# Optimization experiments

Measured on AMD Instinct MI355X. Metric: run time of the kernel, lower is better.

## Reference

```python
import jax, jax.numpy as jnp
import numpy as np

B, S, D, H, FF = 2, 2048, 1024, 16, 4096
DH = D // H
EPS = 1e-5


def rmsnorm(x, g):
    rms = jnp.sqrt(jnp.mean(x * x, axis=-1, keepdims=True) + EPS)
    return x / rms * g


def gelu(x):
    return x * 0.5 * (1.0 + jax.lax.erf(x / np.float32(np.sqrt(2.0))))


def setup_inputs() -> dict:
    key = jax.random.key(0)
    ks = jax.random.split(key, 9)
    sd = np.float32(1.0 / np.sqrt(D))
    sf = np.float32(1.0 / np.sqrt(FF))
    return {
        'x': jax.random.normal(ks[0], (B, S, D), jnp.float32),
        'wq': jax.random.normal(ks[1], (D, D), jnp.float32) * sd,
        'wk': jax.random.normal(ks[2], (D, D), jnp.float32) * sd,
        'wv': jax.random.normal(ks[3], (D, D), jnp.float32) * sd,
        'wo': jax.random.normal(ks[4], (D, D), jnp.float32) * sd,
        'w1': jax.random.normal(ks[5], (FF, D), jnp.float32) * sd,
        'w2': jax.random.normal(ks[6], (D, FF), jnp.float32) * sf,
        'g1': jax.random.uniform(ks[7], (D,), jnp.float32),
        'g2': jax.random.uniform(ks[8], (D,), jnp.float32),
    }


def reference(x, wq, wk, wv, wo, w1, w2, g1, g2):
    b, s, d = x.shape
    h = rmsnorm(x, g1)
    # torch Linear: y = x @ W.T ; split heads -> [b, s, H, DH]
    q = jnp.einsum('bsd,ed->bse', h, wq).reshape(b, s, H, DH)
    k = jnp.einsum('bsd,ed->bse', h, wk).reshape(b, s, H, DH)
    v = jnp.einsum('bsd,ed->bse', h, wv).reshape(b, s, H, DH)
    score = jnp.einsum('bqhd,bkhd->bhqk', q, k) / np.float32(np.sqrt(DH))
    causal = jnp.triu(jnp.ones((s, s), bool), 1)  # strictly upper = masked
    score = score + jnp.where(causal, jnp.float32(-1e9), jnp.float32(0.0))
    attn_w = jax.nn.softmax(score, axis=-1)
    o = jnp.einsum('bhqk,bkhd->bqhd', attn_w, v).reshape(b, s, d)
    attn_out = jnp.einsum('bsd,ed->bse', o, wo)
    x2 = attn_out + x
    h2 = rmsnorm(x2, g2)
    ffn = jnp.einsum('bsf,df->bsd', gelu(jnp.einsum('bsd,fd->bsf', h2, w1)), w2)
    return ffn + x2
```

## Files before the change

### kernel.cpp

```cpp
#include <hip/hip_runtime.h>
#include <cstdint>

#define B_ 2
#define S_ 2048
#define D_ 1024
#define H_ 16
#define DH_ 64
#define FF_ 4096
#define M_TOK (B_ * S_)

typedef __attribute__((ext_vector_type(8))) short short8;
typedef __attribute__((ext_vector_type(4))) float f32x4;
typedef __attribute__((ext_vector_type(4))) unsigned short us4;

typedef unsigned short u16;

__device__ __forceinline__ float bf2f(u16 u) {
  union { uint32_t u; float f; } x;
  x.u = ((uint32_t)u) << 16;
  return x.f;
}
__device__ __forceinline__ u16 f2bf(float f) {
  union { float f; uint32_t u; } x;
  x.f = f;
  uint32_t r = x.u + 0x7FFFu + ((x.u >> 16) & 1u);
  return (u16)(r >> 16);
}

__device__ __forceinline__ void gl_lds16(const void* g, void* l) {
  __builtin_amdgcn_global_load_lds(
      (const __attribute__((address_space(1))) uint32_t*)(uintptr_t)g,
      (__attribute__((address_space(3))) uint32_t*)(uintptr_t)l, 16, 0, 0);
}

__device__ __forceinline__ float gelu_f(float v) {
  const float y = 0.7978845608f * (v + 0.044715f * v * v * v);
  const float t = exp2f(y * 2.885390082f);
  const float th = 1.0f - 2.0f * __builtin_amdgcn_rcpf(t + 1.0f);
  return 0.5f * v * (1.0f + th);
}

#define MEG 1048576
__global__ __launch_bounds__(256) void cvt_all_k(const float* __restrict__ wq, const float* __restrict__ wk,
                                                 const float* __restrict__ wv, const float* __restrict__ wo,
                                                 const float* __restrict__ w1, const float* __restrict__ w2,
                                                 u16* __restrict__ wqkv, u16* __restrict__ wob,
                                                 u16* __restrict__ w1b, u16* __restrict__ w2b) {
  const int n = (blockIdx.x * 256 + threadIdx.x) * 4;
  const float* src;
  u16* dst;
  int off;
  if (n < 3 * MEG) {
    dst = wqkv; off = n;
    src = (n < MEG) ? wq + n : (n < 2 * MEG ? wk + (n - MEG) : wv + (n - 2 * MEG));
  } else if (n < 4 * MEG) {
    dst = wob; off = n - 3 * MEG; src = wo + off;
  } else if (n < 8 * MEG) {
    dst = w1b; off = n - 4 * MEG; src = w1 + off;
  } else {
    dst = w2b; off = n - 8 * MEG; src = w2 + off;
  }
  const float4 v = *(const float4*)src;
  us4 o;
  o[0] = f2bf(v.x); o[1] = f2bf(v.y); o[2] = f2bf(v.z); o[3] = f2bf(v.w);
  *(us4*)&dst[off] = o;
}

__global__ __launch_bounds__(256) void zero_k(float* __restrict__ Of, float* __restrict__ L) {
  const int i = (blockIdx.x * 256 + threadIdx.x) * 4;
  if (i < 4 * MEG) { *(float4*)&Of[i] = float4{0.f, 0.f, 0.f, 0.f}; }
  else { *(float4*)&L[i - 4 * MEG] = float4{0.f, 0.f, 0.f, 0.f}; }
}

__global__ __launch_bounds__(256) void norm_o_k(const float* __restrict__ Of, const float* __restrict__ L,
                                                u16* __restrict__ O) {
  const int row = blockIdx.x;
  const int tid = threadIdx.x;
  const int col = tid * 4;
  const int hh = col >> 6;
  const float lv = L[(size_t)((row >> 11) * 16 + hh) * 2048 + (row & 2047)];
  const float inv = 1.0f / lv;
  const float4 v = *(const float4*)&Of[(size_t)row * D_ + col];
  us4 o;
  o[0] = f2bf(v.x * inv); o[1] = f2bf(v.y * inv);
  o[2] = f2bf(v.z * inv); o[3] = f2bf(v.w * inv);
  *(us4*)&O[(size_t)row * D_ + col] = o;
}

__global__ __launch_bounds__(256) void rmsnorm_k(const float* __restrict__ X,
                                                 const float* __restrict__ G,
                                                 u16* __restrict__ Hout) {
  const int row = blockIdx.x;
  const int tid = threadIdx.x;
  const float4 xx = *(const float4*)&X[(size_t)row * D_ + tid * 4];
  float v[4] = {xx.x, xx.y, xx.z, xx.w};
  float s = 0.f;
#pragma unroll
  for (int i = 0; i < 4; ++i) s += v[i] * v[i];
#pragma unroll
  for (int d = 1; d < 64; d <<= 1) s += __shfl_xor(s, d);
  __shared__ float red[4];
  if ((tid & 63) == 0) red[tid >> 6] = s;
  __syncthreads();
  s = red[0] + red[1] + red[2] + red[3];
  const float scale = rsqrtf(s * (1.0f / (float)D_) + 1e-5f);
  const float4 gg = *(const float4*)&G[tid * 4];
  us4 o;
  o[0] = f2bf(v[0] * scale * gg.x);
  o[1] = f2bf(v[1] * scale * gg.y);
  o[2] = f2bf(v[2] * scale * gg.z);
  o[3] = f2bf(v[3] * scale * gg.w);
  *(us4*)&Hout[(size_t)row * D_ + tid * 4] = o;
}

__global__ __launch_bounds__(256) void rmsnorm_wo_k(const u16* __restrict__ P0, const u16* __restrict__ P1,
                                                    const float* __restrict__ X, const float* __restrict__ G,
                                                    float* __restrict__ X2, u16* __restrict__ Hout) {
  const int row = blockIdx.x;
  const int tid = threadIdx.x;
  const size_t off = (size_t)row * D_ + tid * 4;
  const us4 p0 = *(const us4*)&P0[off];
  const us4 p1 = *(const us4*)&P1[off];
  const float4 xx = *(const float4*)&X[off];
  float v[4];
  v[0] = bf2f(p0[0]) + bf2f(p1[0]) + xx.x;
  v[1] = bf2f(p0[1]) + bf2f(p1[1]) + xx.y;
  v[2] = bf2f(p0[2]) + bf2f(p1[2]) + xx.z;
  v[3] = bf2f(p0[3]) + bf2f(p1[3]) + xx.w;
  *(float4*)&X2[off] = float4{v[0], v[1], v[2], v[3]};
  float s = 0.f;
#pragma unroll
  for (int i = 0; i < 4; ++i) s += v[i] * v[i];
#pragma unroll
  for (int d = 1; d < 64; d <<= 1) s += __shfl_xor(s, d);
  __shared__ float red[4];
  if ((tid & 63) == 0) red[tid >> 6] = s;
  __syncthreads();
  s = red[0] + red[1] + red[2] + red[3];
  const float scale = rsqrtf(s * (1.0f / (float)D_) + 1e-5f);
  const float4 gg = *(const float4*)&G[tid * 4];
  us4 o;
  o[0] = f2bf(v[0] * scale * gg.x);
  o[1] = f2bf(v[1] * scale * gg.y);
  o[2] = f2bf(v[2] * scale * gg.z);
  o[3] = f2bf(v[3] * scale * gg.w);
  *(us4*)&Hout[off] = o;
}

__global__ __launch_bounds__(256) void ffn2_red_k(const u16* __restrict__ Q0, const u16* __restrict__ Q1,
                                                  float* __restrict__ OUT) {
  const int i = (blockIdx.x * 256 + threadIdx.x) * 4;
  const us4 a = *(const us4*)&Q0[i];
  const us4 b = *(const us4*)&Q1[i];
  const float4 c = *(const float4*)&OUT[i];
  *(float4*)&OUT[i] = float4{bf2f(a[0]) + bf2f(b[0]) + c.x, bf2f(a[1]) + bf2f(b[1]) + c.y,
                             bf2f(a[2]) + bf2f(b[2]) + c.z, bf2f(a[3]) + bf2f(b[3]) + c.w};
}

template <int MODE>
__global__ __launch_bounds__(256) void gemm_bt_k(const u16* __restrict__ A,
                                                 const u16* __restrict__ W,
                                                 u16* __restrict__ C0, u16* __restrict__ C1,
                                                 u16* __restrict__ C2, int N, int K) {
  __shared__ alignas(16) u16 As[128 * 32];
  __shared__ alignas(16) u16 Bs[128 * 32];
  const int tid = threadIdx.x;
  const int wv = tid >> 6, lane = tid & 63;
  const int r = lane & 15, quad = lane >> 4;
  const int bm = blockIdx.y * 128, bn = blockIdx.x * 128;
  const int row0 = (wv >> 1) * 64, col0 = (wv & 1) * 64;

  f32x4 acc[4][4] = {};

  int srow[2], sg[2];
#pragma unroll
  for (int jj = 0; jj < 2; ++jj) {
    const int c = wv * 128 + jj * 64 + lane;
    srow[jj] = c >> 2;
    sg[jj] = (c & 3) ^ ((srow[jj] >> 1) & 3);
  }

  for (int k0 = 0; k0 < K; k0 += 32) {
#pragma unroll
    for (int jj = 0; jj < 2; ++jj) {
      const int l0 = (wv * 128 + jj * 64) * 8;
      gl_lds16(&A[(size_t)(bm + srow[jj]) * K + k0 + sg[jj] * 8], &As[l0]);
      gl_lds16(&W[(size_t)(bn + srow[jj]) * K + k0 + sg[jj] * 8], &Bs[l0]);
    }
    __syncthreads();
    short8 af[4], bf[4];
#pragma unroll
    for (int mt = 0; mt < 4; ++mt) {
      const int mr = row0 + mt * 16 + r;
      af[mt] = *(const short8*)&As[mr * 32 + (quad ^ ((mr >> 1) & 3)) * 8];
    }
#pragma unroll
    for (int nt = 0; nt < 4; ++nt) {
      const int nr = col0 + nt * 16 + r;
      bf[nt] = *(const short8*)&Bs[nr * 32 + (quad ^ ((nr >> 1) & 3)) * 8];
    }
#pragma unroll
    for (int mt = 0; mt < 4; ++mt)
#pragma unroll
      for (int nt = 0; nt < 4; ++nt)
        acc[mt][nt] = __builtin_amdgcn_mfma_f32_16x16x32_bf16(af[mt], bf[nt], acc[mt][nt], 0, 0, 0);
    __syncthreads();
  }

  if constexpr (MODE == 2) {
#pragma unroll
    for (int mt = 0; mt < 4; ++mt)
#pragma unroll
      for (int nt = 0; nt < 4; ++nt)
#pragma unroll
        for (int i = 0; i < 4; ++i) {
          const int grow = bm + row0 + mt * 16 + quad * 4 + i;
          const int gcol = bn + col0 + nt * 16 + r;
          C0[(size_t)grow * N + gcol] = f2bf(gelu_f(acc[mt][nt][i]));
        }
  } else {
#pragma unroll
    for (int mt = 0; mt < 4; ++mt) {
      const int grow0 = bm + row0 + mt * 16 + quad * 4;
#pragma unroll
      for (int nt = 0; nt < 4; ++nt) {
        const int gcol = bn + col0 + nt * 16 + r;
        if (gcol < 2048) {
          u16* dst = (gcol < 1024) ? C0 : C1;
          const int cc = gcol & 1023;
#pragma unroll
          for (int i = 0; i < 4; ++i)
            dst[(size_t)(grow0 + i) * 1024 + cc] = f2bf(acc[mt][nt][i]);
        } else {
          const int vcol = gcol - 2048;
          us4 o;
#pragma unroll
          for (int i = 0; i < 4; ++i) o[i] = f2bf(acc[mt][nt][i]);
          const size_t addr =
              ((size_t)((grow0 >> 11) * 16 + (vcol >> 6)) * 64 + (vcol & 63)) * 2048 + (grow0 & 2047);
          *(us4*)&C2[addr] = o;
        }
      }
    }
  }
}

__global__ __launch_bounds__(256) void gemm_sk2_k(const u16* __restrict__ A,
                                                  const u16* __restrict__ W,
                                                  u16* __restrict__ P0, u16* __restrict__ P1,
                                                  int N, int K, int KS) {
  __shared__ alignas(16) u16 As[128 * 32];
  __shared__ alignas(16) u16 Bs[128 * 32];
  const int tid = threadIdx.x;
  const int wv = tid >> 6, lane = tid & 63;
  const int r = lane & 15, quad = lane >> 4;
  const int bm = blockIdx.y * 128, bn = blockIdx.x * 128;
  const int row0 = (wv >> 1) * 64, col0 = (wv & 1) * 64;
  const int koff = blockIdx.z * KS;
  u16* P = blockIdx.z ? P1 : P0;

  f32x4 acc[4][4] = {};

  int srow[2], sg[2];
#pragma unroll
  for (int jj = 0; jj < 2; ++jj) {
    const int c = wv * 128 + jj * 64 + lane;
    srow[jj] = c >> 2;
    sg[jj] = (c & 3) ^ ((srow[jj] >> 1) & 3);
  }

  for (int k0 = koff; k0 < koff + KS; k0 += 32) {
#pragma unroll
    for (int jj = 0; jj < 2; ++jj) {
      const int l0 = (wv * 128 + jj * 64) * 8;
      gl_lds16(&A[(size_t)(bm + srow[jj]) * K + k0 + sg[jj] * 8], &As[l0]);
      gl_lds16(&W[(size_t)(bn + srow[jj]) * K + k0 + sg[jj] * 8], &Bs[l0]);
    }
    __syncthreads();
    short8 af[4], bf[4];
#pragma unroll
    for (int mt = 0; mt < 4; ++mt) {
      const int mr = row0 + mt * 16 + r;
      af[mt] = *(const short8*)&As[mr * 32 + (quad ^ ((mr >> 1) & 3)) * 8];
    }
#pragma unroll
    for (int nt = 0; nt < 4; ++nt) {
      const int nr = col0 + nt * 16 + r;
      bf[nt] = *(const short8*)&Bs[nr * 32 + (quad ^ ((nr >> 1) & 3)) * 8];
    }
#pragma unroll
    for (int mt = 0; mt < 4; ++mt)
#pragma unroll
      for (int nt = 0; nt < 4; ++nt)
        acc[mt][nt] = __builtin_amdgcn_mfma_f32_16x16x32_bf16(af[mt], bf[nt], acc[mt][nt], 0, 0, 0);
    __syncthreads();
  }

#pragma unroll
  for (int mt = 0; mt < 4; ++mt)
#pragma unroll
    for (int nt = 0; nt < 4; ++nt)
#pragma unroll
      for (int i = 0; i < 4; ++i) {
        const int grow = bm + row0 + mt * 16 + quad * 4 + i;
        const int gcol = bn + col0 + nt * 16 + r;
        P[(size_t)grow * N + gcol] = f2bf(acc[mt][nt][i]);
      }
}

#define SCL 0.18033688011112042f
__global__ __launch_bounds__(256, 2) void attn_k(const u16* __restrict__ Q,
                                                 const u16* __restrict__ Kx,
                                                 const u16* __restrict__ VT,
                                                 float* __restrict__ Of, float* __restrict__ L) {
  __shared__ alignas(16) u16 Ks[2][32 * 72];
  __shared__ alignas(16) u16 Vs[2][64 * 40];
  __shared__ alignas(16) u16 Ps[4][32 * 40];

  const int tid = threadIdx.x;
  const int wv = tid >> 6, lane = tid & 63;
  const int r = lane & 15, quad = lane >> 4;
  const int bh = blockIdx.y;
  const int b = bh >> 4, hh = bh & 15;

  int id = 39 - (int)blockIdx.x;
  int bx = 0;
  for (;;) {
    const int nb = (bx >> 2) + 1;
    if (id < nb) break;
    id -= nb;
    ++bx;
  }
  const int c = id;
  const int j0base = c * 512;
  const int niter = (min(bx * 128 + 128, j0base + 512) - j0base) >> 5;

  const int qbase = bx * 128;
  const int m0 = qbase + wv * 32;
  const size_t base = (size_t)b * S_ * D_ + (size_t)hh * DH_;
  const u16* Qb = Q + base;
  const u16* Kb = Kx + base;
  const u16* VTb = VT + (size_t)bh * 64 * 2048;
  u16* Psw = &Ps[wv][0];

  short8 qf[2][2];
#pragma unroll
  for (int f = 0; f < 2; ++f) {
    qf[f][0] = *(const short8*)&Qb[(size_t)(m0 + f * 16 + r) * D_ + quad * 8];
    qf[f][1] = *(const short8*)&Qb[(size_t)(m0 + f * 16 + r) * D_ + 32 + quad * 8];
  }

  short8 onesv;
#pragma unroll
  for (int e = 0; e < 8; ++e) onesv[e] = (short)0x3F80;

  f32x4 oacc[2][4] = {};
  f32x4 lacc[2] = {};

  const int krow = tid >> 3, kg = tid & 7;
  const int vrow = tid >> 2, vg = tid & 3;

  *(short8*)&Ks[0][krow * 72 + kg * 8] = *(const short8*)&Kb[(size_t)(j0base + krow) * D_ + kg * 8];
  *(short8*)&Vs[0][vrow * 40 + vg * 8] = *(const short8*)&VTb[(size_t)vrow * 2048 + j0base + vg * 8];

  int cur = 0;
  for (int it = 0; it < niter; ++it) {
    const int j0 = j0base + it * 32;
    __syncthreads();

    if (it + 1 < niter) {
      const int j1 = j0 + 32;
      *(short8*)&Ks[cur ^ 1][krow * 72 + kg * 8] =
          *(const short8*)&Kb[(size_t)(j1 + krow) * D_ + kg * 8];
      *(short8*)&Vs[cur ^ 1][vrow * 40 + vg * 8] =
          *(const short8*)&VTb[(size_t)vrow * 2048 + j1 + vg * 8];
    }

    f32x4 z[2][2];
#pragma unroll
    for (int kt = 0; kt < 2; ++kt) {
      const short8 kf0 = *(const short8*)&Ks[cur][(kt * 16 + r) * 72 + quad * 8];
      const short8 kf1 = *(const short8*)&Ks[cur][(kt * 16 + r) * 72 + 32 + quad * 8];
#pragma unroll
      for (int f = 0; f < 2; ++f) {
        f32x4 zz = {};
        zz = __builtin_amdgcn_mfma_f32_16x16x32_bf16(qf[f][0], kf0, zz, 0, 0, 0);
        zz = __builtin_amdgcn_mfma_f32_16x16x32_bf16(qf[f][1], kf1, zz, 0, 0, 0);
        z[f][kt] = zz;
      }
    }

    const bool masked = (j0 + 31 > m0);
#pragma unroll
    for (int f = 0; f < 2; ++f)
#pragma unroll
      for (int i = 0; i < 4; ++i) {
        const int qrow = m0 + f * 16 + quad * 4 + i;
        float v0 = z[f][0][i] * SCL;
        float v1 = z[f][1][i] * SCL;
        if (masked) {
          if (j0 + r > qrow) v0 = -128.f;
          if (j0 + 16 + r > qrow) v1 = -128.f;
        }
        Psw[(f * 16 + quad * 4 + i) * 40 + r] = f2bf(exp2f(v0));
        Psw[(f * 16 + quad * 4 + i) * 40 + 16 + r] = f2bf(exp2f(v1));
      }

    asm volatile("s_waitcnt lgkmcnt(0)" ::: "memory");

    short8 vf[4];
#pragma unroll
    for (int nt = 0; nt < 4; ++nt)
      vf[nt] = *(const short8*)&Vs[cur][(nt * 16 + r) * 40 + quad * 8];
#pragma unroll
    for (int f = 0; f < 2; ++f) {
      const short8 pf = *(const short8*)&Psw[(f * 16 + r) * 40 + quad * 8];
#pragma unroll
      for (int nt = 0; nt < 4; ++nt)
        oacc[f][nt] = __builtin_amdgcn_mfma_f32_16x16x32_bf16(pf, vf[nt], oacc[f][nt], 0, 0, 0);
      lacc[f] = __builtin_amdgcn_mfma_f32_16x16x32_bf16(pf, onesv, lacc[f], 0, 0, 0);
    }

    cur ^= 1;
  }

#pragma unroll
  for (int f = 0; f < 2; ++f) {
#pragma unroll
    for (int i = 0; i < 4; ++i) {
      const int qrow = m0 + f * 16 + quad * 4 + i;
#pragma unroll
      for (int nt = 0; nt < 4; ++nt)
        atomicAdd(&Of[base + (size_t)qrow * D_ + nt * 16 + r], oacc[f][nt][i]);
      if (r == 0) atomicAdd(&L[(size_t)bh * 2048 + qrow], lacc[f][i]);
    }
  }
}

extern "C" void kernel_launch(void* const* d_in, const int* in_sizes, int n_in,
                              void* d_out, int out_size, void* d_ws, size_t ws_size,
                              hipStream_t stream) {
  (void)in_sizes; (void)n_in; (void)out_size; (void)ws_size;
  const float* x   = (const float*)d_in[0];
  const float* wq  = (const float*)d_in[1];
  const float* wk  = (const float*)d_in[2];
  const float* wvp = (const float*)d_in[3];
  const float* wo  = (const float*)d_in[4];
  const float* w1  = (const float*)d_in[5];
  const float* w2  = (const float*)d_in[6];
  const float* g1  = (const float*)d_in[7];
  const float* g2  = (const float*)d_in[8];
  float* out = (float*)d_out;

  u16* ws = (u16*)d_ws;
  const size_t TD = (size_t)M_TOK * D_;
  u16* h    = ws;
  u16* q    = ws + 1 * TD;
  u16* k    = ws + 2 * TD;
  u16* vt   = ws + 3 * TD;
  u16* h2   = ws + 4 * TD;
  float* l  = (float*)(ws + 4 * TD);
  u16* o    = h;
  u16* t    = ws;
  u16* P0   = q;
  u16* P1   = k;
  u16* Q0   = h2;
  u16* wqkv = ws + 5 * TD;
  u16* wob  = wqkv + 3 * MEG;
  u16* w1b  = wob + 1 * MEG;
  u16* w2b  = w1b + 4 * MEG;
  u16* Q1   = w2b + 4 * MEG;

  const dim3 blk(256);

  cvt_all_k<<<12288, blk, 0, stream>>>(wq, wk, wvp, wo, w1, w2, wqkv, wob, w1b, w2b);
  zero_k<<<(4 * MEG + 65536) / 1024, blk, 0, stream>>>(out, l);
  rmsnorm_k<<<M_TOK, blk, 0, stream>>>(x, g1, h);
  gemm_bt_k<4><<<dim3(24, 32), blk, 0, stream>>>(h, wqkv, q, k, vt, 3072, 1024);
  attn_k<<<dim3(40, 32), blk, 0, stream>>>(q, k, vt, out, l);
  norm_o_k<<<M_TOK, blk, 0, stream>>>(out, l, o);
  gemm_sk2_k<<<dim3(8, 32, 2), blk, 0, stream>>>(o, wob, P0, P1, 1024, 1024, 512);
  rmsnorm_wo_k<<<M_TOK, blk, 0, stream>>>(P0, P1, x, g2, out, h2);
  gemm_bt_k<2><<<dim3(32, 32), blk, 0, stream>>>(h2, w1b, t, nullptr, nullptr, 4096, 1024);
  gemm_sk2_k<<<dim3(8, 32, 2), blk, 0, stream>>>(t, w2b, Q0, Q1, 1024, 4096, 2048);
  ffn2_red_k<<<4096, blk, 0, stream>>>(Q0, Q1, out);
}
```

Measured before the change: 374.0 us.

## Swizzle workgroup order across XCDs, fold softmax scale into Q, tune attention

Remaps block IDs in both GEMMs and in attention so that consecutive workgroups, which the hardware spreads round-robin over the XCDs, land on tiles that share data and reuse L2. Folds the softmax scale into the Q projection epilogue so the attention loop skips one multiply per score. In attention, packs P writes as interleaved bf16 pairs with a matching interleaved V load, so the K-dimension ordering of P and V stays consistent while LDS store count drops. It also raises the occupancy hint to 4 and adds s_setprio around the MFMA sections. The higher occupancy hint can force register spills, and the interleaved V layout must match P exactly to stay correct.

```diff
diff --git a/kernel.cpp b/kernel.cpp
--- a/kernel.cpp
+++ b/kernel.cpp
@@ -14,6 +14,8 @@
 typedef __attribute__((ext_vector_type(4))) unsigned short us4;
 
 typedef unsigned short u16;
+
+#define SCL 0.18033688011112042f
 
 __device__ __forceinline__ float bf2f(u16 u) {
   union { uint32_t u; float f; } x;
@@ -167,7 +169,12 @@
   const int tid = threadIdx.x;
   const int wv = tid >> 6, lane = tid & 63;
   const int r = lane & 15, quad = lane >> 4;
-  const int bm = blockIdx.y * 128, bn = blockIdx.x * 128;
+  const int nx = gridDim.x;
+  const int nwg = nx * gridDim.y;
+  const int orig = blockIdx.x + nx * blockIdx.y;
+  const int id = (orig & 7) * (nwg >> 3) + (orig >> 3);
+  const int bn = (id % nx) * 128;
+  const int bm = (id / nx) * 128;
   const int row0 = (wv >> 1) * 64, col0 = (wv & 1) * 64;
 
   f32x4 acc[4][4] = {};
@@ -227,10 +234,11 @@
         const int gcol = bn + col0 + nt * 16 + r;
         if (gcol < 2048) {
           u16* dst = (gcol < 1024) ? C0 : C1;
+          const float sc = (gcol < 1024) ? SCL : 1.0f;
           const int cc = gcol & 1023;
 #pragma unroll
           for (int i = 0; i < 4; ++i)
-            dst[(size_t)(grow0 + i) * 1024 + cc] = f2bf(acc[mt][nt][i]);
+            dst[(size_t)(grow0 + i) * 1024 + cc] = f2bf(acc[mt][nt][i] * sc);
         } else {
           const int vcol = gcol - 2048;
           us4 o;
@@ -254,10 +262,14 @@
   const int tid = threadIdx.x;
   const int wv = tid >> 6, lane = tid & 63;
   const int r = lane & 15, quad = lane >> 4;
-  const int bm = blockIdx.y * 128, bn = blockIdx.x * 128;
+  const int orig = blockIdx.x + 8 * (blockIdx.y + 32 * blockIdx.z);
+  const int id = (orig & 7) * 64 + (orig >> 3);
+  const int bn = (id & 7) * 128;
+  const int bm = ((id >> 3) & 31) * 128;
+  const int bz = id >> 8;
   const int row0 = (wv >> 1) * 64, col0 = (wv & 1) * 64;
-  const int koff = blockIdx.z * KS;
-  u16* P = blockIdx.z ? P1 : P0;
+  const int koff = bz * KS;
+  u16* P = bz ? P1 : P0;
 
   f32x4 acc[4][4] = {};
 
@@ -308,8 +320,7 @@
       }
 }
 
-#define SCL 0.18033688011112042f
-__global__ __launch_bounds__(256, 2) void attn_k(const u16* __restrict__ Q,
+__global__ __launch_bounds__(256, 4) void attn_k(const u16* __restrict__ Q,
                                                  const u16* __restrict__ Kx,
                                                  const u16* __restrict__ VT,
                                                  float* __restrict__ Of, float* __restrict__ L) {
@@ -320,10 +331,14 @@
   const int tid = threadIdx.x;
   const int wv = tid >> 6, lane = tid & 63;
   const int r = lane & 15, quad = lane >> 4;
-  const int bh = blockIdx.y;
+
+  const int orig = blockIdx.x + 40 * blockIdx.y;
+  const int sid = (orig & 7) * 160 + (orig >> 3);
+  const int sx = sid % 40;
+  const int bh = sid / 40;
   const int b = bh >> 4, hh = bh & 15;
 
-  int id = 39 - (int)blockIdx.x;
+  int id = 39 - sx;
   int bx = 0;
   for (;;) {
     const int nb = (bx >> 2) + 1;
@@ -361,7 +376,15 @@
   const int vrow = tid >> 2, vg = tid & 3;
 
   *(short8*)&Ks[0][krow * 72 + kg * 8] = *(const short8*)&Kb[(size_t)(j0base + krow) * D_ + kg * 8];
-  *(short8*)&Vs[0][vrow * 40 + vg * 8] = *(const short8*)&VTb[(size_t)vrow * 2048 + j0base + vg * 8];
+  {
+    const u16* vsrc = &VTb[(size_t)vrow * 2048 + j0base];
+    const us4 va = *(const us4*)&vsrc[vg * 4];
+    const us4 vb = *(const us4*)&vsrc[vg * 4 + 16];
+    short8 o;
+    o[0] = va[0]; o[1] = vb[0]; o[2] = va[1]; o[3] = vb[1];
+    o[4] = va[2]; o[5] = vb[2]; o[6] = va[3]; o[7] = vb[3];
+    *(short8*)&Vs[0][vrow * 40 + vg * 8] = o;
+  }
 
   int cur = 0;
   for (int it = 0; it < niter; ++it) {
@@ -372,11 +395,17 @@
       const int j1 = j0 + 32;
       *(short8*)&Ks[cur ^ 1][krow * 72 + kg * 8] =
           *(const short8*)&Kb[(size_t)(j1 + krow) * D_ + kg * 8];
-      *(short8*)&Vs[cur ^ 1][vrow * 40 + vg * 8] =
-          *(const short8*)&VTb[(size_t)vrow * 2048 + j1 + vg * 8];
+      const u16* vsrc = &VTb[(size_t)vrow * 2048 + j1];
+      const us4 va = *(const us4*)&vsrc[vg * 4];
+      const us4 vb = *(const us4*)&vsrc[vg * 4 + 16];
+      short8 o;
+      o[0] = va[0]; o[1] = vb[0]; o[2] = va[1]; o[3] = vb[1];
+      o[4] = va[2]; o[5] = vb[2]; o[6] = va[3]; o[7] = vb[3];
+      *(short8*)&Vs[cur ^ 1][vrow * 40 + vg * 8] = o;
     }
 
     f32x4 z[2][2];
+    __builtin_amdgcn_s_setprio(1);
 #pragma unroll
     for (int kt = 0; kt < 2; ++kt) {
       const short8 kf0 = *(const short8*)&Ks[cur][(kt * 16 + r) * 72 + quad * 8];
@@ -389,6 +418,7 @@
         z[f][kt] = zz;
       }
     }
+    __builtin_amdgcn_s_setprio(0);
 
     const bool masked = (j0 + 31 > m0);
 #pragma unroll
@@ -396,14 +426,16 @@
 #pragma unroll
       for (int i = 0; i < 4; ++i) {
         const int qrow = m0 + f * 16 + quad * 4 + i;
-        float v0 = z[f][0][i] * SCL;
-        float v1 = z[f][1][i] * SCL;
+        float v0 = z[f][0][i];
+        float v1 = z[f][1][i];
         if (masked) {
           if (j0 + r > qrow) v0 = -128.f;
           if (j0 + 16 + r > qrow) v1 = -128.f;
         }
-        Psw[(f * 16 + quad * 4 + i) * 40 + r] = f2bf(exp2f(v0));
-        Psw[(f * 16 + quad * 4 + i) * 40 + 16 + r] = f2bf(exp2f(v1));
+        const float e0 = exp2f(v0);
+        const float e1 = exp2f(v1);
+        const uint32_t pk = (uint32_t)f2bf(e0) | ((uint32_t)f2bf(e1) << 16);
+        *(uint32_t*)&Psw[(f * 16 + quad * 4 + i) * 40 + r * 2] = pk;
       }
 
     asm volatile("s_waitcnt lgkmcnt(0)" ::: "memory");
@@ -412,6 +444,7 @@
 #pragma unroll
     for (int nt = 0; nt < 4; ++nt)
       vf[nt] = *(const short8*)&Vs[cur][(nt * 16 + r) * 40 + quad * 8];
+    __builtin_amdgcn_s_setprio(1);
 #pragma unroll
     for (int f = 0; f < 2; ++f) {
       const short8 pf = *(const short8*)&Psw[(f * 16 + r) * 40 + quad * 8];
@@ -420,6 +453,7 @@
         oacc[f][nt] = __builtin_amdgcn_mfma_f32_16x16x32_bf16(pf, vf[nt], oacc[f][nt], 0, 0, 0);
       lacc[f] = __builtin_amdgcn_mfma_f32_16x16x32_bf16(pf, onesv, lacc[f], 0, 0, 0);
     }
+    __builtin_amdgcn_s_setprio(0);
 
     cur ^= 1;
   }
```

Measured after the change: 378.7 us. No clear change (+1.3%).
